# Optimization experiments

Hardware: AMD Instinct MI355X
Metric: run time of the kernel (lower is better)

The kernel has to match this reference:

```python
import jax, jax.numpy as jnp
import numpy as np

CHANNELS = 256
LAYERS = 4
IN_FEAT = 118
N_NODES = 20000
N_EDGES = 320000


def setup_inputs() -> dict:
    key = jax.random.key(0)
    ks = jax.random.split(key, 4 + 4 * LAYERS)
    x = jax.random.normal(ks[0], (N_NODES, IN_FEAT), dtype=jnp.float32)
    edge_index = jax.random.randint(ks[1], (2, N_EDGES), 0, N_NODES, dtype=jnp.int64)
    s = 1.0 / np.sqrt(CHANNELS)
    W_embed = jax.random.normal(ks[2], (IN_FEAT, CHANNELS), dtype=jnp.float32) / np.sqrt(IN_FEAT)
    b_embed = jnp.zeros((CHANNELS,), dtype=jnp.float32)
    W1 = jax.random.normal(ks[3], (LAYERS, CHANNELS, CHANNELS), dtype=jnp.float32) * s
    b1 = jnp.zeros((LAYERS, CHANNELS), dtype=jnp.float32)
    W2 = jax.random.normal(ks[4], (LAYERS, CHANNELS, CHANNELS), dtype=jnp.float32) * s
    b2 = jnp.zeros((LAYERS, CHANNELS), dtype=jnp.float32)
    return {"x": x, "edge_index": edge_index, "W_embed": W_embed, "b_embed": b_embed,
            "W1": W1, "b1": b1, "W2": W2, "b2": b2}


def reference(x, edge_index, W_embed, b_embed, W1, b1, W2, b2):
    n = x.shape[0]
    src, dst = edge_index[0], edge_index[1]
    # in-degree for mean aggregation (constant across layers)
    cnt = jax.ops.segment_sum(jnp.ones(src.shape[0], dtype=x.dtype), dst, num_segments=n)
    inv_cnt = (1.0 / jnp.maximum(cnt, 1.0))[:, None]
    h = x @ W_embed + b_embed  # [N, C]
    for l in range(W1.shape[0]):
        # message: gather source features, dense + exact GELU (dropout off in eval)
        msg = jax.nn.gelu(h[src] @ W1[l] + b1[l], approximate=False)  # [E, C]
        # mean-scatter aggregate over destination nodes
        agg = jax.ops.segment_sum(msg, dst, num_segments=n) * inv_cnt  # [N, C]
        # update: dense + GELU
        h = jax.nn.gelu(agg @ W2[l] + b2[l], approximate=False)
    return jnp.mean(h, axis=1)  # [N]
```

## Files before the change

kernel.cpp:

```cpp
#include <hip/hip_runtime.h>
#include <math.h>

#define CH 256

typedef _Float16 half8 __attribute__((ext_vector_type(8)));
typedef float f32x4 __attribute__((ext_vector_type(4)));

__device__ __forceinline__ float gelu_exact(float v) {
    return 0.5f * v * (1.0f + erff(v * 0.70710678118654752f));
}

__global__ void wsplit_kernel(const float* __restrict__ W1, const float* __restrict__ W2,
                              _Float16* __restrict__ WThi, _Float16* __restrict__ WTlo) {
    int idx = blockIdx.x * blockDim.x + threadIdx.x;
    int n   = idx & 255;
    int kg  = (idx >> 8) & 31;
    int mat = idx >> 13;
    const float* W = (mat < 4) ? (W1 + (size_t)mat * 65536)
                               : (W2 + (size_t)(mat - 4) * 65536);
    _Float16 hi[8], lo[8];
#pragma unroll
    for (int j = 0; j < 8; j++) {
        float v = W[(size_t)(kg * 8 + j) * CH + n];
        _Float16 h = (_Float16)v;
        hi[j] = h;
        lo[j] = (_Float16)(v - (float)h);
    }
    size_t off = (size_t)mat * 65536 + (size_t)n * 256 + kg * 8;
    *(half8*)(WThi + off) = *(half8*)&hi[0];
    *(half8*)(WTlo + off) = *(half8*)&lo[0];
}

__global__ __launch_bounds__(256, 4) void mgemm_kernel(
    const float* __restrict__ A,
    const _Float16* __restrict__ Bhi_g,
    const _Float16* __restrict__ Blo_g,
    const float* __restrict__ bias,
    float* __restrict__ out,
    int M)
{
    __shared__ _Float16 Ah[128][40], Al[128][40], Bh[64][40], Bl[64][40];

    int tid  = threadIdx.x;
    int lane = tid & 63;
    int wave = tid >> 6;
    int wr = wave >> 1;
    int wc = wave & 1;
    int m0 = blockIdx.x * 128;
    int n0 = blockIdx.y * 64;

    f32x4 acc[4][2];
#pragma unroll
    for (int i = 0; i < 4; i++)
#pragma unroll
        for (int j = 0; j < 2; j++) acc[i][j] = (f32x4){0.f, 0.f, 0.f, 0.f};

    const int s_row  = tid >> 1;
    const int s_ch   = (tid & 1) * 16;
    const int s_grow = min(m0 + s_row, M - 1);
    const int bcol = (tid & 127) >> 1;
    const int bch  = (tid & 1) * 16;

    for (int kt = 0; kt < 8; kt++) {
        int k0 = kt * 32;
        {
            const float* src = A + (size_t)s_grow * CH + k0 + s_ch;
            float f[16];
            *(float4*)&f[0]  = ((const float4*)src)[0];
            *(float4*)&f[4]  = ((const float4*)src)[1];
            *(float4*)&f[8]  = ((const float4*)src)[2];
            *(float4*)&f[12] = ((const float4*)src)[3];
            _Float16 hi[16], lo[16];
#pragma unroll
            for (int j = 0; j < 16; j++) {
                _Float16 hh = (_Float16)f[j];
                hi[j] = hh;
                lo[j] = (_Float16)(f[j] - (float)hh);
            }
            *(half8*)&Ah[s_row][s_ch]     = *(half8*)&hi[0];
            *(half8*)&Ah[s_row][s_ch + 8] = *(half8*)&hi[8];
            *(half8*)&Al[s_row][s_ch]     = *(half8*)&lo[0];
            *(half8*)&Al[s_row][s_ch + 8] = *(half8*)&lo[8];
        }
        {
            const _Float16* bs = ((tid < 128) ? Bhi_g : Blo_g)
                                 + (size_t)(n0 + bcol) * 256 + k0 + bch;
            half8 u0 = ((const half8*)bs)[0];
            half8 u1 = ((const half8*)bs)[1];
            _Float16 (*dst)[40] = (tid < 128) ? Bh : Bl;
            *(half8*)&dst[bcol][bch]     = u0;
            *(half8*)&dst[bcol][bch + 8] = u1;
        }
        __syncthreads();

        {
            int frow = lane & 15;
            int fk   = (lane >> 4) * 8;
            half8 ah[4], al[4], bh[2], bl[2];
#pragma unroll
            for (int rf = 0; rf < 4; rf++) {
                int r = wr * 64 + rf * 16 + frow;
                ah[rf] = *(const half8*)&Ah[r][fk];
                al[rf] = *(const half8*)&Al[r][fk];
            }
#pragma unroll
            for (int cf = 0; cf < 2; cf++) {
                int c = wc * 32 + cf * 16 + frow;
                bh[cf] = *(const half8*)&Bh[c][fk];
                bl[cf] = *(const half8*)&Bl[c][fk];
            }
#pragma unroll
            for (int rf = 0; rf < 4; rf++)
#pragma unroll
                for (int cf = 0; cf < 2; cf++) {
                    acc[rf][cf] = __builtin_amdgcn_mfma_f32_16x16x32_f16(ah[rf], bh[cf], acc[rf][cf], 0, 0, 0);
                    acc[rf][cf] = __builtin_amdgcn_mfma_f32_16x16x32_f16(ah[rf], bl[cf], acc[rf][cf], 0, 0, 0);
                    acc[rf][cf] = __builtin_amdgcn_mfma_f32_16x16x32_f16(al[rf], bh[cf], acc[rf][cf], 0, 0, 0);
                }
        }
        __syncthreads();
    }

    int ccol = lane & 15;
    int crow = (lane >> 4) * 4;
#pragma unroll
    for (int cf = 0; cf < 2; cf++) {
        int gcol = n0 + wc * 32 + cf * 16 + ccol;
        float bb = bias[gcol];
#pragma unroll
        for (int rf = 0; rf < 4; rf++) {
#pragma unroll
            for (int q = 0; q < 4; q++) {
                int grow = m0 + wr * 64 + rf * 16 + crow + q;
                if (grow < M)
                    out[(size_t)grow * CH + gcol] = gelu_exact(acc[rf][cf][q] + bb);
            }
        }
    }
}

template<bool DOGELU>
__global__ __launch_bounds__(256) void gemm_kernel(const float* __restrict__ A,
                                                   const float* __restrict__ W,
                                                   const float* __restrict__ bias,
                                                   float* __restrict__ out,
                                                   int M, int K)
{
    const int BM = 128, BN = 64, BK = 64;
    __shared__ float As[BK][BM + 4];
    __shared__ float Bs[BK][BN + 4];

    int tid = threadIdx.x;
    int m0 = blockIdx.x * BM;
    int n0 = blockIdx.y * BN;
    int ty = tid >> 4;
    int tx = tid & 15;

    float acc[8][4];
#pragma unroll
    for (int i = 0; i < 8; i++)
#pragma unroll
        for (int j = 0; j < 4; j++) acc[i][j] = 0.f;

    const int s_arow = tid >> 2;
    const int s_akq  = tid & 3;
    const int s_bk   = tid >> 4;
    const int s_bc   = (tid & 15) * 4;
    const bool kalign = ((K & 3) == 0);

    for (int k0 = 0; k0 < K; k0 += BK) {
        const bool fullk = kalign && (k0 + BK <= K);
#pragma unroll
        for (int it = 0; it < 2; it++) {
            int row = it * 64 + s_arow;
            int grow = min(m0 + row, M - 1);
            const float* src = A + (size_t)grow * K;
            if (fullk) {
                int kb = k0 + s_akq * 16;
                float4 v0 = *(const float4*)(src + kb);
                float4 v1 = *(const float4*)(src + kb + 4);
                float4 v2 = *(const float4*)(src + kb + 8);
                float4 v3 = *(const float4*)(src + kb + 12);
                int kr = s_akq * 16;
                As[kr +  0][row] = v0.x; As[kr +  1][row] = v0.y;
                As[kr +  2][row] = v0.z; As[kr +  3][row] = v0.w;
                As[kr +  4][row] = v1.x; As[kr +  5][row] = v1.y;
                As[kr +  6][row] = v1.z; As[kr +  7][row] = v1.w;
                As[kr +  8][row] = v2.x; As[kr +  9][row] = v2.y;
                As[kr + 10][row] = v2.z; As[kr + 11][row] = v2.w;
                As[kr + 12][row] = v3.x; As[kr + 13][row] = v3.y;
                As[kr + 14][row] = v3.z; As[kr + 15][row] = v3.w;
            } else {
#pragma unroll
                for (int q = 0; q < 16; q++) {
                    int k = k0 + s_akq * 16 + q;
                    As[s_akq * 16 + q][row] = (k < K) ? src[min(k, K - 1)] : 0.f;
                }
            }
        }
#pragma unroll
        for (int it = 0; it < 4; it++) {
            int kr = it * 16 + s_bk;
            int gk = k0 + kr;
            float4 v = {0.f, 0.f, 0.f, 0.f};
            if (gk < K) v = *(const float4*)(W + (size_t)gk * CH + n0 + s_bc);
            *(float4*)&Bs[kr][s_bc] = v;
        }
        __syncthreads();

#pragma unroll 16
        for (int kk = 0; kk < BK; kk++) {
            float a[8], b[4];
            *(float4*)&a[0] = *(const float4*)&As[kk][ty * 8];
            *(float4*)&a[4] = *(const float4*)&As[kk][ty * 8 + 4];
            *(float4*)&b[0] = *(const float4*)&Bs[kk][tx * 4];
#pragma unroll
            for (int i = 0; i < 8; i++)
#pragma unroll
                for (int j = 0; j < 4; j++)
                    acc[i][j] = fmaf(a[i], b[j], acc[i][j]);
        }
        __syncthreads();
    }

    float b4[4];
    *(float4*)&b4[0] = *(const float4*)(bias + n0 + tx * 4);
#pragma unroll
    for (int i = 0; i < 8; i++) {
        int row = m0 + ty * 8 + i;
        if (row < M) {
            float o[4];
#pragma unroll
            for (int j = 0; j < 4; j++) {
                float v = acc[i][j] + b4[j];
                o[j] = DOGELU ? gelu_exact(v) : v;
            }
            *(float4*)(out + (size_t)row * CH + n0 + tx * 4) = *(float4*)&o[0];
        }
    }
}

__global__ void zero_int_kernel(int* p, int n) {
    int i = blockIdx.x * blockDim.x + threadIdx.x;
    if (i < n) p[i] = 0;
}

__global__ void degree_kernel(const int* __restrict__ ei, int E, int* deg) {
    int e = blockIdx.x * blockDim.x + threadIdx.x;
    if (e < E) atomicAdd(&deg[ei[E + e]], 1);
}

__global__ void scan_part_kernel(const int* __restrict__ deg, int* bsum, int N) {
    int t = threadIdx.x;
    int base = blockIdx.x * 1024 + t * 4;
    int4 v = {0, 0, 0, 0};
    if (base + 3 < N) v = *(const int4*)(deg + base);
    else {
        if (base + 0 < N) v.x = deg[base + 0];
        if (base + 1 < N) v.y = deg[base + 1];
        if (base + 2 < N) v.z = deg[base + 2];
        if (base + 3 < N) v.w = deg[base + 3];
    }
    __shared__ int sh[256];
    sh[t] = v.x + v.y + v.z + v.w;
    __syncthreads();
    for (int off = 128; off; off >>= 1) {
        if (t < off) sh[t] += sh[t + off];
        __syncthreads();
    }
    if (t == 0) bsum[blockIdx.x] = sh[0];
}

__global__ void scan_top_kernel(const int* __restrict__ bsum, int* boff, int B) {
    __shared__ int sh[256];
    int t = threadIdx.x;
    int own = (t < B) ? bsum[t] : 0;
    sh[t] = own;
    __syncthreads();
    for (int off = 1; off < 256; off <<= 1) {
        int v = (t >= off) ? sh[t - off] : 0;
        __syncthreads();
        sh[t] += v;
        __syncthreads();
    }
    if (t < B) boff[t] = sh[t] - own;
}

__global__ void scan_final_kernel(const int* __restrict__ deg, const int* __restrict__ boff,
                                  int* row_ptr, int* fill_pos, float* inv, int N, int E) {
    int t = threadIdx.x;
    int base = blockIdx.x * 1024 + t * 4;
    int4 v = {0, 0, 0, 0};
    if (base + 3 < N) v = *(const int4*)(deg + base);
    else {
        if (base + 0 < N) v.x = deg[base + 0];
        if (base + 1 < N) v.y = deg[base + 1];
        if (base + 2 < N) v.z = deg[base + 2];
        if (base + 3 < N) v.w = deg[base + 3];
    }
    int own = v.x + v.y + v.z + v.w;
    __shared__ int sh[256];
    sh[t] = own;
    __syncthreads();
    for (int off = 1; off < 256; off <<= 1) {
        int s = (t >= off) ? sh[t - off] : 0;
        __syncthreads();
        sh[t] += s;
        __syncthreads();
    }
    int run = boff[blockIdx.x] + (sh[t] - own);
    int4 rp;
    rp.x = run;
    rp.y = run + v.x;
    rp.z = rp.y + v.y;
    rp.w = rp.z + v.z;
    if (base + 3 < N) {
        *(int4*)(row_ptr + base) = rp;
        *(int4*)(fill_pos + base) = rp;
        float4 iv;
        iv.x = 1.0f / fmaxf((float)v.x, 1.0f);
        iv.y = 1.0f / fmaxf((float)v.y, 1.0f);
        iv.z = 1.0f / fmaxf((float)v.z, 1.0f);
        iv.w = 1.0f / fmaxf((float)v.w, 1.0f);
        *(float4*)(inv + base) = iv;
    } else {
        int rr[4] = {rp.x, rp.y, rp.z, rp.w};
        int dd[4] = {v.x, v.y, v.z, v.w};
        for (int q = 0; q < 4; q++) {
            if (base + q < N) {
                row_ptr[base + q] = rr[q];
                fill_pos[base + q] = rr[q];
                inv[base + q] = 1.0f / fmaxf((float)dd[q], 1.0f);
            }
        }
    }
    if (blockIdx.x == 0 && t == 0) row_ptr[N] = E;
}

__global__ void fill_kernel(const int* __restrict__ ei, int E, int* fill_pos, int* colv) {
    int e = blockIdx.x * blockDim.x + threadIdx.x;
    if (e < E) {
        int p = atomicAdd(&fill_pos[ei[E + e]], 1);
        colv[p] = ei[e];
    }
}

__global__ void agg_kernel(const float* __restrict__ t, const int* __restrict__ row_ptr,
                           const int* __restrict__ colv, const float* __restrict__ inv,
                           float* __restrict__ agg, int N) {
    int n = blockIdx.x * 4 + (threadIdx.x >> 6);
    if (n >= N) return;
    int lane = threadIdx.x & 63;
    int s = row_ptr[n], e = row_ptr[n + 1];
    size_t loff = (size_t)lane * 4;

    f32x4 a0 = {0.f, 0.f, 0.f, 0.f}, a1 = a0, a2 = a0, a3 = a0;
    int j = s;
    for (; j + 4 <= e; j += 4) {
        int c0 = colv[j], c1 = colv[j + 1], c2 = colv[j + 2], c3 = colv[j + 3];
        const float4* p0 = (const float4*)(t + (size_t)c0 * CH + loff);
        const float4* p1 = (const float4*)(t + (size_t)c1 * CH + loff);
        const float4* p2 = (const float4*)(t + (size_t)c2 * CH + loff);
        const float4* p3 = (const float4*)(t + (size_t)c3 * CH + loff);
        float4 v0 = *p0; float4 v1 = *p1; float4 v2 = *p2; float4 v3 = *p3;
        a0 += (f32x4){v0.x, v0.y, v0.z, v0.w};
        a1 += (f32x4){v1.x, v1.y, v1.z, v1.w};
        a2 += (f32x4){v2.x, v2.y, v2.z, v2.w};
        a3 += (f32x4){v3.x, v3.y, v3.z, v3.w};
    }
    for (; j < e; j++) {
        float4 v = *(const float4*)(t + (size_t)colv[j] * CH + loff);
        a0 += (f32x4){v.x, v.y, v.z, v.w};
    }
    f32x4 tot = (a0 + a1) + (a2 + a3);
    float sc = inv[n];
    float o[4] = {tot[0] * sc, tot[1] * sc, tot[2] * sc, tot[3] * sc};
    *(float4*)(agg + (size_t)n * CH + loff) = *(float4*)&o[0];
}

__global__ void mean_kernel(const float* __restrict__ h, float* __restrict__ out, int N) {
    int n = blockIdx.x * 4 + (threadIdx.x >> 6);
    if (n >= N) return;
    int lane = threadIdx.x & 63;
    float4 v = *(const float4*)(h + (size_t)n * CH + lane * 4);
    float s = v.x + v.y + v.z + v.w;
#pragma unroll
    for (int off = 32; off; off >>= 1) s += __shfl_down(s, off, 64);
    if (lane == 0) out[n] = s * (1.0f / 256.0f);
}

extern "C" void kernel_launch(void* const* d_in, const int* in_sizes, int n_in,
                              void* d_out, int out_size, void* d_ws, size_t ws_size,
                              hipStream_t stream) {
    const float* x       = (const float*)d_in[0];
    const int*   ei      = (const int*)d_in[1];
    const float* W_embed = (const float*)d_in[2];
    const float* b_embed = (const float*)d_in[3];
    const float* W1      = (const float*)d_in[4];
    const float* b1      = (const float*)d_in[5];
    const float* W2      = (const float*)d_in[6];
    const float* b2      = (const float*)d_in[7];
    float* out = (float*)d_out;

    int N = in_sizes[0] / 118;
    int E = in_sizes[1] / 2;
    int SB = (N + 1023) / 1024;

    float*     h        = (float*)d_ws;
    float*     t        = h + (size_t)N * CH;
    float*     agg      = t + (size_t)N * CH;
    _Float16*  WThi     = (_Float16*)(agg + (size_t)N * CH);
    _Float16*  WTlo     = WThi + 8 * 65536;
    float*     inv      = (float*)(WTlo + 8 * 65536);
    int*       deg      = (int*)(inv + N);
    int*       row_ptr  = deg + N;
    int*       fill_pos = row_ptr + (N + 1);
    int*       colv     = fill_pos + N;
    int*       bsum     = colv + E;
    int*       boff     = bsum + 256;

    zero_int_kernel<<<(N + 255) / 256, 256, 0, stream>>>(deg, N);
    degree_kernel<<<(E + 255) / 256, 256, 0, stream>>>(ei, E, deg);
    scan_part_kernel<<<SB, 256, 0, stream>>>(deg, bsum, N);
    scan_top_kernel<<<1, 256, 0, stream>>>(bsum, boff, SB);
    scan_final_kernel<<<SB, 256, 0, stream>>>(deg, boff, row_ptr, fill_pos, inv, N, E);
    fill_kernel<<<(E + 255) / 256, 256, 0, stream>>>(ei, E, fill_pos, colv);
    wsplit_kernel<<<256, 256, 0, stream>>>(W1, W2, WThi, WTlo);

    dim3 gg((N + 127) / 128, 4);
    gemm_kernel<false><<<gg, 256, 0, stream>>>(x, W_embed, b_embed, h, N, 118);

    dim3 mg((N + 127) / 128, 4);
    for (int l = 0; l < 4; l++) {
        mgemm_kernel<<<mg, 256, 0, stream>>>(h, WThi + (size_t)l * 65536,
                                             WTlo + (size_t)l * 65536,
                                             b1 + (size_t)l * CH, t, N);
        agg_kernel<<<(N + 3) / 4, 256, 0, stream>>>(t, row_ptr, colv, inv, agg, N);
        mgemm_kernel<<<mg, 256, 0, stream>>>(agg, WThi + (size_t)(4 + l) * 65536,
                                             WTlo + (size_t)(4 + l) * 65536,
                                             b2 + (size_t)l * CH, h, N);
    }
    mean_kernel<<<(N + 3) / 4, 256, 0, stream>>>(h, out, N);
}
```

Measured before the change: 468.6 us.

## Store activations as pre-split fp16 hi/lo pairs and use MFMA for embedding

Intermediate activations are now stored as hi/lo fp16 pairs produced in GEMM and aggregation epilogues, so the MFMA GEMM no longer converts fp32 A tiles on load. The scalar fp32 embedding GEMM is replaced by the split-fp16 MFMA kernel over K padded to 128, fed by new x and W_embed split kernels. Byte traffic per activation is unchanged, but each element now needs two separate 2-byte loads in the gather and GEMM paths. The epilogue also issues scalar 2-byte stores, which may coalesce poorly.

Result: slower. 482.7 us (+3.0%).

```diff
diff --git a/kernel.cpp b/kernel.cpp
--- a/kernel.cpp
+++ b/kernel.cpp
@@ -4,6 +4,7 @@
 #define CH 256
 
 typedef _Float16 half8 __attribute__((ext_vector_type(8)));
+typedef _Float16 half4 __attribute__((ext_vector_type(4)));
 typedef float f32x4 __attribute__((ext_vector_type(4)));
 
 __device__ __forceinline__ float gelu_exact(float v) {
@@ -31,14 +32,55 @@
     *(half8*)(WTlo + off) = *(half8*)&lo[0];
 }
 
+__global__ void wesplit_kernel(const float* __restrict__ We,
+                               _Float16* __restrict__ WeTh, _Float16* __restrict__ WeTl) {
+    int idx = blockIdx.x * blockDim.x + threadIdx.x;
+    if (idx >= 4096) return;
+    int n  = idx >> 4;
+    int k8 = (idx & 15) * 8;
+    _Float16 hi[8], lo[8];
+#pragma unroll
+    for (int j = 0; j < 8; j++) {
+        int k = k8 + j;
+        float v = (k < 118) ? We[(size_t)k * CH + n] : 0.f;
+        _Float16 h = (_Float16)v;
+        hi[j] = h;
+        lo[j] = (_Float16)(v - (float)h);
+    }
+    size_t off = (size_t)n * 128 + k8;
+    *(half8*)(WeTh + off) = *(half8*)&hi[0];
+    *(half8*)(WeTl + off) = *(half8*)&lo[0];
+}
+
+__global__ void xsplit_kernel(const float* __restrict__ x,
+                              _Float16* __restrict__ xh, _Float16* __restrict__ xl, int N) {
+    int idx = blockIdx.x * blockDim.x + threadIdx.x;
+    int n  = idx >> 4;
+    int c8 = (idx & 15) * 8;
+    if (n >= N) return;
+    _Float16 hi[8], lo[8];
+#pragma unroll
+    for (int j = 0; j < 8; j++) {
+        int c = c8 + j;
+        float v = (c < 118) ? x[(size_t)n * 118 + c] : 0.f;
+        _Float16 h = (_Float16)v;
+        hi[j] = h;
+        lo[j] = (_Float16)(v - (float)h);
+    }
+    size_t off = (size_t)n * 128 + c8;
+    *(half8*)(xh + off) = *(half8*)&hi[0];
+    *(half8*)(xl + off) = *(half8*)&lo[0];
+}
+
+template<int KT, bool DOGELU>
 __global__ __launch_bounds__(256, 4) void mgemm_kernel(
-    const float* __restrict__ A,
-    const _Float16* __restrict__ Bhi_g,
-    const _Float16* __restrict__ Blo_g,
+    const _Float16* __restrict__ Ah_g, const _Float16* __restrict__ Al_g,
+    const _Float16* __restrict__ Bh_g, const _Float16* __restrict__ Bl_g,
     const float* __restrict__ bias,
-    float* __restrict__ out,
+    _Float16* __restrict__ Oh, _Float16* __restrict__ Ol,
     int M)
 {
+    const int KLEN = KT * 32;
     __shared__ _Float16 Ah[128][40], Al[128][40], Bh[64][40], Bl[64][40];
 
     int tid  = threadIdx.x;
@@ -55,36 +97,29 @@
 #pragma unroll
         for (int j = 0; j < 2; j++) acc[i][j] = (f32x4){0.f, 0.f, 0.f, 0.f};
 
-    const int s_row  = tid >> 1;
-    const int s_ch   = (tid & 1) * 16;
-    const int s_grow = min(m0 + s_row, M - 1);
+    const int s_row = tid >> 1;
+    const int s_ch  = (tid & 1) * 16;
+    const size_t s_arow = (size_t)min(m0 + s_row, M - 1);
     const int bcol = (tid & 127) >> 1;
     const int bch  = (tid & 1) * 16;
 
-    for (int kt = 0; kt < 8; kt++) {
+    for (int kt = 0; kt < KT; kt++) {
         int k0 = kt * 32;
         {
-            const float* src = A + (size_t)s_grow * CH + k0 + s_ch;
-            float f[16];
-            *(float4*)&f[0]  = ((const float4*)src)[0];
-            *(float4*)&f[4]  = ((const float4*)src)[1];
-            *(float4*)&f[8]  = ((const float4*)src)[2];
-            *(float4*)&f[12] = ((const float4*)src)[3];
-            _Float16 hi[16], lo[16];
-#pragma unroll
-            for (int j = 0; j < 16; j++) {
-                _Float16 hh = (_Float16)f[j];
-                hi[j] = hh;
-                lo[j] = (_Float16)(f[j] - (float)hh);
-            }
-            *(half8*)&Ah[s_row][s_ch]     = *(half8*)&hi[0];
-            *(half8*)&Ah[s_row][s_ch + 8] = *(half8*)&hi[8];
-            *(half8*)&Al[s_row][s_ch]     = *(half8*)&lo[0];
-            *(half8*)&Al[s_row][s_ch + 8] = *(half8*)&lo[8];
+            const _Float16* sh_ = Ah_g + s_arow * KLEN + k0 + s_ch;
+            const _Float16* sl_ = Al_g + s_arow * KLEN + k0 + s_ch;
+            half8 h0 = ((const half8*)sh_)[0];
+            half8 h1 = ((const half8*)sh_)[1];
+            half8 l0 = ((const half8*)sl_)[0];
+            half8 l1 = ((const half8*)sl_)[1];
+            *(half8*)&Ah[s_row][s_ch]     = h0;
+            *(half8*)&Ah[s_row][s_ch + 8] = h1;
+            *(half8*)&Al[s_row][s_ch]     = l0;
+            *(half8*)&Al[s_row][s_ch + 8] = l1;
         }
         {
-            const _Float16* bs = ((tid < 128) ? Bhi_g : Blo_g)
-                                 + (size_t)(n0 + bcol) * 256 + k0 + bch;
+            const _Float16* bs = ((tid < 128) ? Bh_g : Bl_g)
+                                 + (size_t)(n0 + bcol) * KLEN + k0 + bch;
             half8 u0 = ((const half8*)bs)[0];
             half8 u1 = ((const half8*)bs)[1];
             _Float16 (*dst)[40] = (tid < 128) ? Bh : Bl;
@@ -132,110 +167,14 @@
 #pragma unroll
             for (int q = 0; q < 4; q++) {
                 int grow = m0 + wr * 64 + rf * 16 + crow + q;
-                if (grow < M)
-                    out[(size_t)grow * CH + gcol] = gelu_exact(acc[rf][cf][q] + bb);
-            }
-        }
-    }
-}
-
-template<bool DOGELU>
-__global__ __launch_bounds__(256) void gemm_kernel(const float* __restrict__ A,
-                                                   const float* __restrict__ W,
-                                                   const float* __restrict__ bias,
-                                                   float* __restrict__ out,
-                                                   int M, int K)
-{
-    const int BM = 128, BN = 64, BK = 64;
-    __shared__ float As[BK][BM + 4];
-    __shared__ float Bs[BK][BN + 4];
-
-    int tid = threadIdx.x;
-    int m0 = blockIdx.x * BM;
-    int n0 = blockIdx.y * BN;
-    int ty = tid >> 4;
-    int tx = tid & 15;
-
-    float acc[8][4];
-#pragma unroll
-    for (int i = 0; i < 8; i++)
-#pragma unroll
-        for (int j = 0; j < 4; j++) acc[i][j] = 0.f;
-
-    const int s_arow = tid >> 2;
-    const int s_akq  = tid & 3;
-    const int s_bk   = tid >> 4;
-    const int s_bc   = (tid & 15) * 4;
-    const bool kalign = ((K & 3) == 0);
-
-    for (int k0 = 0; k0 < K; k0 += BK) {
-        const bool fullk = kalign && (k0 + BK <= K);
-#pragma unroll
-        for (int it = 0; it < 2; it++) {
-            int row = it * 64 + s_arow;
-            int grow = min(m0 + row, M - 1);
-            const float* src = A + (size_t)grow * K;
-            if (fullk) {
-                int kb = k0 + s_akq * 16;
-                float4 v0 = *(const float4*)(src + kb);
-                float4 v1 = *(const float4*)(src + kb + 4);
-                float4 v2 = *(const float4*)(src + kb + 8);
-                float4 v3 = *(const float4*)(src + kb + 12);
-                int kr = s_akq * 16;
-                As[kr +  0][row] = v0.x; As[kr +  1][row] = v0.y;
-                As[kr +  2][row] = v0.z; As[kr +  3][row] = v0.w;
-                As[kr +  4][row] = v1.x; As[kr +  5][row] = v1.y;
-                As[kr +  6][row] = v1.z; As[kr +  7][row] = v1.w;
-                As[kr +  8][row] = v2.x; As[kr +  9][row] = v2.y;
-                As[kr + 10][row] = v2.z; As[kr + 11][row] = v2.w;
-                As[kr + 12][row] = v3.x; As[kr + 13][row] = v3.y;
-                As[kr + 14][row] = v3.z; As[kr + 15][row] = v3.w;
-            } else {
-#pragma unroll
-                for (int q = 0; q < 16; q++) {
-                    int k = k0 + s_akq * 16 + q;
-                    As[s_akq * 16 + q][row] = (k < K) ? src[min(k, K - 1)] : 0.f;
+                if (grow < M) {
+                    float v = acc[rf][cf][q] + bb;
+                    float g = DOGELU ? gelu_exact(v) : v;
+                    _Float16 hi = (_Float16)g;
+                    Oh[(size_t)grow * CH + gcol] = hi;
+                    Ol[(size_t)grow * CH + gcol] = (_Float16)(g - (float)hi);
                 }
             }
-        }
-#pragma unroll
-        for (int it = 0; it < 4; it++) {
-            int kr = it * 16 + s_bk;
-            int gk = k0 + kr;
-            float4 v = {0.f, 0.f, 0.f, 0.f};
-            if (gk < K) v = *(const float4*)(W + (size_t)gk * CH + n0 + s_bc);
-            *(float4*)&Bs[kr][s_bc] = v;
-        }
-        __syncthreads();
-
-#pragma unroll 16
-        for (int kk = 0; kk < BK; kk++) {
-            float a[8], b[4];
-            *(float4*)&a[0] = *(const float4*)&As[kk][ty * 8];
-            *(float4*)&a[4] = *(const float4*)&As[kk][ty * 8 + 4];
-            *(float4*)&b[0] = *(const float4*)&Bs[kk][tx * 4];
-#pragma unroll
-            for (int i = 0; i < 8; i++)
-#pragma unroll
-                for (int j = 0; j < 4; j++)
-                    acc[i][j] = fmaf(a[i], b[j], acc[i][j]);
-        }
-        __syncthreads();
-    }
-
-    float b4[4];
-    *(float4*)&b4[0] = *(const float4*)(bias + n0 + tx * 4);
-#pragma unroll
-    for (int i = 0; i < 8; i++) {
-        int row = m0 + ty * 8 + i;
-        if (row < M) {
-            float o[4];
-#pragma unroll
-            for (int j = 0; j < 4; j++) {
-                float v = acc[i][j] + b4[j];
-                o[j] = DOGELU ? gelu_exact(v) : v;
-            }
-            *(float4*)(out + (size_t)row * CH + n0 + tx * 4) = *(float4*)&o[0];
         }
     }
 }
@@ -345,9 +284,10 @@
     }
 }
 
-__global__ void agg_kernel(const float* __restrict__ t, const int* __restrict__ row_ptr,
-                           const int* __restrict__ colv, const float* __restrict__ inv,
-                           float* __restrict__ agg, int N) {
+__global__ void agg_kernel(const _Float16* __restrict__ th, const _Float16* __restrict__ tl,
+                           const int* __restrict__ row_ptr, const int* __restrict__ colv,
+                           const float* __restrict__ inv,
+                           _Float16* __restrict__ aggh, _Float16* __restrict__ aggl, int N) {
     int n = blockIdx.x * 4 + (threadIdx.x >> 6);
     if (n >= N) return;
     int lane = threadIdx.x & 63;
@@ -358,32 +298,53 @@
     int j = s;
     for (; j + 4 <= e; j += 4) {
         int c0 = colv[j], c1 = colv[j + 1], c2 = colv[j + 2], c3 = colv[j + 3];
-        const float4* p0 = (const float4*)(t + (size_t)c0 * CH + loff);
-        const float4* p1 = (const float4*)(t + (size_t)c1 * CH + loff);
-        const float4* p2 = (const float4*)(t + (size_t)c2 * CH + loff);
-        const float4* p3 = (const float4*)(t + (size_t)c3 * CH + loff);
-        float4 v0 = *p0; float4 v1 = *p1; float4 v2 = *p2; float4 v3 = *p3;
-        a0 += (f32x4){v0.x, v0.y, v0.z, v0.w};
-        a1 += (f32x4){v1.x, v1.y, v1.z, v1.w};
-        a2 += (f32x4){v2.x, v2.y, v2.z, v2.w};
-        a3 += (f32x4){v3.x, v3.y, v3.z, v3.w};
+        half4 h0 = *(const half4*)(th + (size_t)c0 * CH + loff);
+        half4 l0 = *(const half4*)(tl + (size_t)c0 * CH + loff);
+        half4 h1 = *(const half4*)(th + (size_t)c1 * CH + loff);
+        half4 l1 = *(const half4*)(tl + (size_t)c1 * CH + loff);
+        half4 h2 = *(const half4*)(th + (size_t)c2 * CH + loff);
+        half4 l2 = *(const half4*)(tl + (size_t)c2 * CH + loff);
+        half4 h3 = *(const half4*)(th + (size_t)c3 * CH + loff);
+        half4 l3 = *(const half4*)(tl + (size_t)c3 * CH + loff);
+#pragma unroll
+        for (int q = 0; q < 4; q++) {
+            a0[q] += (float)h0[q] + (float)l0[q];
+            a1[q] += (float)h1[q] + (float)l1[q];
+            a2[q] += (float)h2[q] + (float)l2[q];
+            a3[q] += (float)h3[q] + (float)l3[q];
+        }
     }
     for (; j < e; j++) {
-        float4 v = *(const float4*)(t + (size_t)colv[j] * CH + loff);
-        a0 += (f32x4){v.x, v.y, v.z, v.w};
+        int c = colv[j];
+        half4 h = *(const half4*)(th + (size_t)c * CH + loff);
+        half4 l = *(const half4*)(tl + (size_t)c * CH + loff);
+#pragma unroll
+        for (int q = 0; q < 4; q++) a0[q] += (float)h[q] + (float)l[q];
     }
     f32x4 tot = (a0 + a1) + (a2 + a3);
     float sc = inv[n];
-    float o[4] = {tot[0] * sc, tot[1] * sc, tot[2] * sc, tot[3] * sc};
-    *(float4*)(agg + (size_t)n * CH + loff) = *(float4*)&o[0];
-}
-
-__global__ void mean_kernel(const float* __restrict__ h, float* __restrict__ out, int N) {
+    _Float16 oh[4], ol[4];
+#pragma unroll
+    for (int q = 0; q < 4; q++) {
+        float v = tot[q] * sc;
+        _Float16 hi = (_Float16)v;
+        oh[q] = hi;
+        ol[q] = (_Float16)(v - (float)hi);
+    }
+    *(half4*)(aggh + (size_t)n * CH + loff) = *(half4*)&oh[0];
+    *(half4*)(aggl + (size_t)n * CH + loff) = *(half4*)&ol[0];
+}
+
+__global__ void mean_kernel(const _Float16* __restrict__ hh, const _Float16* __restrict__ hl,
+                            float* __restrict__ out, int N) {
     int n = blockIdx.x * 4 + (threadIdx.x >> 6);
     if (n >= N) return;
     int lane = threadIdx.x & 63;
-    float4 v = *(const float4*)(h + (size_t)n * CH + lane * 4);
-    float s = v.x + v.y + v.z + v.w;
+    half4 vh = *(const half4*)(hh + (size_t)n * CH + lane * 4);
+    half4 vl = *(const half4*)(hl + (size_t)n * CH + lane * 4);
+    float s = 0.f;
+#pragma unroll
+    for (int q = 0; q < 4; q++) s += (float)vh[q] + (float)vl[q];
 #pragma unroll
     for (int off = 32; off; off >>= 1) s += __shfl_down(s, off, 64);
     if (lane == 0) out[n] = s * (1.0f / 256.0f);
@@ -405,19 +366,28 @@
     int N = in_sizes[0] / 118;
     int E = in_sizes[1] / 2;
     int SB = (N + 1023) / 1024;
-
-    float*     h        = (float*)d_ws;
-    float*     t        = h + (size_t)N * CH;
-    float*     agg      = t + (size_t)N * CH;
-    _Float16*  WThi     = (_Float16*)(agg + (size_t)N * CH);
-    _Float16*  WTlo     = WThi + 8 * 65536;
-    float*     inv      = (float*)(WTlo + 8 * 65536);
-    int*       deg      = (int*)(inv + N);
-    int*       row_ptr  = deg + N;
-    int*       fill_pos = row_ptr + (N + 1);
-    int*       colv     = fill_pos + N;
-    int*       bsum     = colv + E;
-    int*       boff     = bsum + 256;
+    size_t NC = (size_t)N * CH;
+
+    _Float16* hh   = (_Float16*)d_ws;
+    _Float16* hl   = hh + NC;
+    _Float16* th   = hl + NC;
+    _Float16* tl   = th + NC;
+    _Float16* ah   = tl + NC;
+    _Float16* al   = ah + NC;
+    _Float16* WThi = al + NC;
+    _Float16* WTlo = WThi + 8 * 65536;
+    _Float16* WeTh = WTlo + 8 * 65536;
+    _Float16* WeTl = WeTh + 256 * 128;
+    float*    inv      = (float*)(WeTl + 256 * 128);
+    int*      deg      = (int*)(inv + N);
+    int*      row_ptr  = deg + N;
+    int*      fill_pos = row_ptr + (N + 1);
+    int*      colv     = fill_pos + N;
+    int*      bsum     = colv + E;
+    int*      boff     = bsum + 256;
+
+    _Float16* xh = th;
+    _Float16* xl = th + (size_t)N * 128;
 
     zero_int_kernel<<<(N + 255) / 256, 256, 0, stream>>>(deg, N);
     degree_kernel<<<(E + 255) / 256, 256, 0, stream>>>(ei, E, deg);
@@ -426,19 +396,22 @@
     scan_final_kernel<<<SB, 256, 0, stream>>>(deg, boff, row_ptr, fill_pos, inv, N, E);
     fill_kernel<<<(E + 255) / 256, 256, 0, stream>>>(ei, E, fill_pos, colv);
     wsplit_kernel<<<256, 256, 0, stream>>>(W1, W2, WThi, WTlo);
-
-    dim3 gg((N + 127) / 128, 4);
-    gemm_kernel<false><<<gg, 256, 0, stream>>>(x, W_embed, b_embed, h, N, 118);
+    wesplit_kernel<<<16, 256, 0, stream>>>(W_embed, WeTh, WeTl);
+    xsplit_kernel<<<(N * 16 + 255) / 256, 256, 0, stream>>>(x, xh, xl, N);
 
     dim3 mg((N + 127) / 128, 4);
+    mgemm_kernel<4, false><<<mg, 256, 0, stream>>>(xh, xl, WeTh, WeTl, b_embed, hh, hl, N);
+
     for (int l = 0; l < 4; l++) {
-        mgemm_kernel<<<mg, 256, 0, stream>>>(h, WThi + (size_t)l * 65536,
-                                             WTlo + (size_t)l * 65536,
-                                             b1 + (size_t)l * CH, t, N);
-        agg_kernel<<<(N + 3) / 4, 256, 0, stream>>>(t, row_ptr, colv, inv, agg, N);
-        mgemm_kernel<<<mg, 256, 0, stream>>>(agg, WThi + (size_t)(4 + l) * 65536,
-                                             WTlo + (size_t)(4 + l) * 65536,
-                                             b2 + (size_t)l * CH, h, N);
-    }
-    mean_kernel<<<(N + 3) / 4, 256, 0, stream>>>(h, out, N);
-}
+        mgemm_kernel<8, true><<<mg, 256, 0, stream>>>(hh, hl,
+                                                      WThi + (size_t)l * 65536,
+                                                      WTlo + (size_t)l * 65536,
+                                                      b1 + (size_t)l * CH, th, tl, N);
+        agg_kernel<<<(N + 3) / 4, 256, 0, stream>>>(th, tl, row_ptr, colv, inv, ah, al, N);
+        mgemm_kernel<8, true><<<mg, 256, 0, stream>>>(ah, al,
+                                                      WThi + (size_t)(4 + l) * 65536,
+                                                      WTlo + (size_t)(4 + l) * 65536,
+                                                      b2 + (size_t)l * CH, hh, hl, N);
+    }
+    mean_kernel<<<(N + 3) / 4, 256, 0, stream>>>(hh, hl, out, N);
+}
```
